# Optimization experiments

Measured on AMD Instinct MI355X. Metric: run time of the kernel, lower is better.

## Reference

```python
import jax, jax.numpy as jnp
import numpy as np
from math import factorial

ZETA = [1, 2, 3, 4]          # configs['zeta']=4 -> range(1,5)
NZETA = len(ZETA)
NRAD = 16
NLAMBDA = 2
NAT = 4000
NEDGE = 100000
ZMAX = max(ZETA)


def _make_lxlylz(zmax):
    tr, fn = [], []
    for s in range(zmax + 1):
        for lx in range(s + 1):
            for ly in range(s - lx + 1):
                lz = s - lx - ly
                tr.append((lx, ly, lz))
                fn.append(factorial(s) / (factorial(lx) * factorial(ly) * factorial(lz)))
    return np.asarray(tr, np.int32), np.asarray(fn, np.float32)


def setup_inputs() -> dict:
    key = jax.random.key(0)
    k1, k2, k3, k4 = jax.random.split(key, 4)
    rij = jax.random.normal(k1, (NEDGE, 3), dtype=jnp.float32)
    rij_unit = rij / jnp.linalg.norm(rij, axis=-1, keepdims=True)
    radial_ij = jax.random.uniform(k2, (NEDGE, NRAD, NZETA + 1), dtype=jnp.float32)
    lambda_weights = jax.random.normal(k3, (NLAMBDA,), dtype=jnp.float32)
    first_atom_idx = jnp.sort(jax.random.randint(k4, (NEDGE,), 0, NAT, dtype=jnp.int32))
    tr, fn = _make_lxlylz(ZMAX)
    return {
        "rij_unit": rij_unit,
        "radial_ij": radial_ij,
        "lambda_weights": lambda_weights,
        "fact_norm": jnp.asarray(fn),
        "first_atom_idx": first_atom_idx,
        "lxlylz": jnp.asarray(tr),
        "lxlylz_sum": jnp.asarray(tr.sum(axis=-1).astype(np.int32)),
        "nat": NAT,
    }


def reference(rij_unit, radial_ij, lambda_weights, fact_norm,
              first_atom_idx, lxlylz, lxlylz_sum, nat):
    # angular monomials g_ij_lxlylz : [E, L]
    lf = lxlylz.astype(jnp.float32)
    g_ij = jnp.prod(rij_unit[:, None, :] ** lf[None, :, :], axis=-1) * fact_norm[None, :]
    # lambda^(lx+ly+lz) : [n_lambda, L]
    lam = lambda_weights[:, None] ** lxlylz_sum.astype(jnp.float32)[None, :]
    # two-body radial descriptor: segment-sum of last radial channel -> [nat, Nrad]
    radial_i = jax.ops.segment_sum(radial_ij[:, :, -1], first_atom_idx, num_segments=nat)
    feats = [radial_i]
    for r_idx, z in enumerate(ZETA):
        # gather-compute: [E, Nrad, L]
        g = jnp.einsum('ej,ek->ejk', radial_ij[:, :, r_idx], g_ij)
        # scatter-reduce over neighbors of each central atom -> [nat, Nrad, L]
        g_i = jax.ops.segment_sum(g, first_atom_idx, num_segments=nat)
        # three-body power contraction with lambda weights, norm 2^(1-z)
        gi3 = jnp.einsum('njk,lk->njl', g_i * g_i, lam) * jnp.float32(2.0 ** (1.0 - z))
        feats.append(gi3.reshape(nat, -1))
    return jnp.concatenate(feats, axis=-1)  # [nat, Nrad*(1 + n_lambda*nzeta)]
```

## Files before the change

kernel.cpp:

```cpp
#include <hip/hip_runtime.h>

#define NRAD 16
#define NCH  5
#define NMON 35
#define OUTW 144
#define ROWF (NRAD * NCH)

__global__ __launch_bounds__(256) void seg_offsets(
    const int* __restrict__ idx, int* __restrict__ seg, int E, int nat)
{
    int e = blockIdx.x * blockDim.x + threadIdx.x;
    if (e >= E) return;
    if (e == 0) {
        const int b = idx[0];
        for (int n = 0; n <= b; ++n) seg[n] = 0;
    } else {
        const int a = idx[e - 1], b = idx[e];
        for (int n = a + 1; n <= b; ++n) seg[n] = e;
    }
    if (e == E - 1) {
        const int a = idx[E - 1];
        for (int n = a + 1; n <= nat; ++n) seg[n] = E;
    }
}

__device__ __forceinline__ void edge_body(
    float x, float y, float z, float rad, float c4,
    float acc[NMON], float& acc2)
{
    const float x2 = x * x, x3 = x2 * x, x4 = x2 * x2;
    const float y2 = y * y, y3 = y2 * y, y4 = y2 * y2;
    const float z2 = z * z, z3 = z2 * z, z4 = z2 * z2;
    const float xy = x * y, xz = x * z, yz = y * z;

    acc2 += c4;
    acc[0]  += rad;
    acc[1]  = fmaf(rad, z,        acc[1]);
    acc[2]  = fmaf(rad, y,        acc[2]);
    acc[3]  = fmaf(rad, x,        acc[3]);
    acc[4]  = fmaf(rad, z2,       acc[4]);
    acc[5]  = fmaf(rad, yz,       acc[5]);
    acc[6]  = fmaf(rad, y2,       acc[6]);
    acc[7]  = fmaf(rad, xz,       acc[7]);
    acc[8]  = fmaf(rad, xy,       acc[8]);
    acc[9]  = fmaf(rad, x2,       acc[9]);
    acc[10] = fmaf(rad, z3,       acc[10]);
    acc[11] = fmaf(rad, y * z2,   acc[11]);
    acc[12] = fmaf(rad, y2 * z,   acc[12]);
    acc[13] = fmaf(rad, y3,       acc[13]);
    acc[14] = fmaf(rad, x * z2,   acc[14]);
    acc[15] = fmaf(rad, xy * z,   acc[15]);
    acc[16] = fmaf(rad, x * y2,   acc[16]);
    acc[17] = fmaf(rad, x2 * z,   acc[17]);
    acc[18] = fmaf(rad, x2 * y,   acc[18]);
    acc[19] = fmaf(rad, x3,       acc[19]);
    acc[20] = fmaf(rad, z4,       acc[20]);
    acc[21] = fmaf(rad, y * z3,   acc[21]);
    acc[22] = fmaf(rad, y2 * z2,  acc[22]);
    acc[23] = fmaf(rad, y3 * z,   acc[23]);
    acc[24] = fmaf(rad, y4,       acc[24]);
    acc[25] = fmaf(rad, x * z3,   acc[25]);
    acc[26] = fmaf(rad, xy * z2,  acc[26]);
    acc[27] = fmaf(rad, x * y2 * z, acc[27]);
    acc[28] = fmaf(rad, x * y3,   acc[28]);
    acc[29] = fmaf(rad, x2 * z2,  acc[29]);
    acc[30] = fmaf(rad, x2 * yz,  acc[30]);
    acc[31] = fmaf(rad, x2 * y2,  acc[31]);
    acc[32] = fmaf(rad, x3 * z,   acc[32]);
    acc[33] = fmaf(rad, x3 * y,   acc[33]);
    acc[34] = fmaf(rad, x4,       acc[34]);
}

__global__ __launch_bounds__(64) void mbp_wave(
    const float* __restrict__ rij_unit,
    const float* __restrict__ radial_ij,
    const float* __restrict__ lambda_w,
    const float* __restrict__ fact_norm,
    const int*   __restrict__ seg,
    float* __restrict__ out)
{
    const int n    = blockIdx.x;
    const int lane = threadIdx.x;
    const int zi   = lane >> 4;
    const int r    = lane & 15;

    const int start = seg[n];
    const int end   = seg[n + 1];

    float acc[NMON];
    #pragma unroll
    for (int l = 0; l < NMON; ++l) acc[l] = 0.f;
    float acc2 = 0.f;

    const int off  = r * NCH + zi;
    const int off4 = r * NCH + 4;

    #pragma unroll 2
    for (int e = start; e < end; ++e) {
        const float* __restrict__ row = radial_ij + (size_t)e * ROWF;
        const float rad = row[off];
        const float c4  = row[off4];
        const float x   = rij_unit[3 * e + 0];
        const float y   = rij_unit[3 * e + 1];
        const float z   = rij_unit[3 * e + 2];
        edge_body(x, y, z, rad, c4, acc, acc2);
    }

    const float l0 = lambda_w[0], l1 = lambda_w[1];
    const float p0[5] = {1.f, l0, l0 * l0, l0 * l0 * l0, (l0 * l0) * (l0 * l0)};
    const float p1[5] = {1.f, l1, l1 * l1, l1 * l1 * l1, (l1 * l1) * (l1 * l1)};
    const int lsum_tab[NMON] = {0, 1,1,1, 2,2,2,2,2,2,
                                3,3,3,3,3,3,3,3,3,3,
                                4,4,4,4,4,4,4,4,4,4,4,4,4,4,4};
    float s0 = 0.f, s1 = 0.f;
    #pragma unroll
    for (int l = 0; l < NMON; ++l) {
        const float v  = acc[l] * fact_norm[l];
        const float v2 = v * v;
        s0 = fmaf(v2, p0[lsum_tab[l]], s0);
        s1 = fmaf(v2, p1[lsum_tab[l]], s1);
    }
    const float scale = 1.0f / (float)(1 << zi);
    float* orow = out + (long)n * OUTW;
    orow[16 + zi * 32 + r * 2 + 0] = s0 * scale;
    orow[16 + zi * 32 + r * 2 + 1] = s1 * scale;
    if (zi == 0) orow[r] = acc2;
}

extern "C" void kernel_launch(void* const* d_in, const int* in_sizes, int n_in,
                              void* d_out, int out_size, void* d_ws, size_t ws_size,
                              hipStream_t stream) {
    const float* rij_unit   = (const float*)d_in[0];
    const float* radial_ij  = (const float*)d_in[1];
    const float* lambda_w   = (const float*)d_in[2];
    const float* fact_norm  = (const float*)d_in[3];
    const int*   first_atom = (const int*)d_in[4];
    const int E   = in_sizes[4];
    const int nat = out_size / OUTW;

    int* seg = (int*)d_ws;

    seg_offsets<<<(E + 255) / 256, 256, 0, stream>>>(first_atom, seg, E, nat);
    mbp_wave<<<nat, 64, 0, stream>>>(rij_unit, radial_ij, lambda_w,
                                     fact_norm, seg, (float*)d_out);
}
```

Measured before the change: 107.3 us.

## Fuse segment-offset computation into main kernel via wave-parallel binary search

Removes the separate seg_offsets kernel and its workspace round trip. Instead, each wavefront finds its atom's edge range directly with a 64-way ballot-based lower-bound search over the sorted first_atom array. This saves one kernel launch and its dependency, at the cost of a few extra dependent global loads per block before accumulation starts. The edge loop unroll is also raised from 2 to 4.

```diff
diff --git a/kernel.cpp b/kernel.cpp
--- a/kernel.cpp
+++ b/kernel.cpp
@@ -5,24 +5,6 @@
 #define NMON 35
 #define OUTW 144
 #define ROWF (NRAD * NCH)
-
-__global__ __launch_bounds__(256) void seg_offsets(
-    const int* __restrict__ idx, int* __restrict__ seg, int E, int nat)
-{
-    int e = blockIdx.x * blockDim.x + threadIdx.x;
-    if (e >= E) return;
-    if (e == 0) {
-        const int b = idx[0];
-        for (int n = 0; n <= b; ++n) seg[n] = 0;
-    } else {
-        const int a = idx[e - 1], b = idx[e];
-        for (int n = a + 1; n <= b; ++n) seg[n] = e;
-    }
-    if (e == E - 1) {
-        const int a = idx[E - 1];
-        for (int n = a + 1; n <= nat; ++n) seg[n] = E;
-    }
-}
 
 __device__ __forceinline__ void edge_body(
     float x, float y, float z, float rad, float c4,
@@ -71,21 +53,41 @@
     acc[34] = fmaf(rad, x4,       acc[34]);
 }
 
-__global__ __launch_bounds__(64) void mbp_wave(
+__device__ __forceinline__ int lb_wave(const int* __restrict__ a, int E,
+                                       int key, int lane)
+{
+    int lo = 0, hi = E;
+    while (hi - lo > 64) {
+        const int step = (hi - lo + 63) >> 6;
+        const int p = lo + lane * step;
+        const int v = (p < hi) ? a[p] : 0x7fffffff;
+        const int k = __popcll(__ballot(v < key));
+        if (k == 0) return lo;
+        const int nlo = lo + (k - 1) * step + 1;
+        const int nhi = min(lo + k * step, hi);
+        lo = nlo; hi = nhi;
+    }
+    const int p = lo + lane;
+    const int v = (p < hi) ? a[p] : 0x7fffffff;
+    return lo + __popcll(__ballot(v < key));
+}
+
+__global__ __launch_bounds__(64) void mbp_fused(
     const float* __restrict__ rij_unit,
     const float* __restrict__ radial_ij,
     const float* __restrict__ lambda_w,
     const float* __restrict__ fact_norm,
-    const int*   __restrict__ seg,
-    float* __restrict__ out)
+    const int*   __restrict__ first_atom,
+    float* __restrict__ out,
+    int E)
 {
     const int n    = blockIdx.x;
     const int lane = threadIdx.x;
     const int zi   = lane >> 4;
     const int r    = lane & 15;
 
-    const int start = seg[n];
-    const int end   = seg[n + 1];
+    const int start = lb_wave(first_atom, E, n, lane);
+    const int end   = lb_wave(first_atom, E, n + 1, lane);
 
     float acc[NMON];
     #pragma unroll
@@ -95,7 +97,7 @@
     const int off  = r * NCH + zi;
     const int off4 = r * NCH + 4;
 
-    #pragma unroll 2
+    #pragma unroll 4
     for (int e = start; e < end; ++e) {
         const float* __restrict__ row = radial_ij + (size_t)e * ROWF;
         const float rad = row[off];
@@ -138,9 +140,6 @@
     const int E   = in_sizes[4];
     const int nat = out_size / OUTW;
 
-    int* seg = (int*)d_ws;
-
-    seg_offsets<<<(E + 255) / 256, 256, 0, stream>>>(first_atom, seg, E, nat);
-    mbp_wave<<<nat, 64, 0, stream>>>(rij_unit, radial_ij, lambda_w,
-                                     fact_norm, seg, (float*)d_out);
+    mbp_fused<<<nat, 64, 0, stream>>>(rij_unit, radial_ij, lambda_w,
+                                      fact_norm, first_atom, (float*)d_out, E);
 }
```

New measurement: 107.3 us. Within noise of the previous version (-0.0%).
